# Optimization experiments

Measured on AMD Instinct MI355X. Metric: run time of the kernel, lower is better.

The kernel has to match this reference:

```python
import jax, jax.numpy as jnp
import numpy as np
from jax import lax

# ---- config (FalconH1Mixer, FalconH1-1.5B-like) ----
BATCH = 2
SEQ = 2048
HID = 2048
EXPAND = 2
INTER = EXPAND * HID          # 4096 (mamba_d_ssm=None)
HEADS = 64
PDIM = INTER // HEADS         # 64 head_dim
NSTATE = 128                  # mamba_d_state
G = 1                         # mamba_n_groups
HPG = HEADS // G
KCONV = 4                     # mamba_d_conv
GTS = G * NSTATE
CONV_DIM = INTER + 2 * GTS    # 4352
PROJ_DIM = 2 * INTER + 2 * GTS + HEADS  # 8512 (z | xBC | dt)
EPS = 1e-5
MUP = (0.25, 0.5, 0.5, 0.5, 1.0)  # ssm_multipliers for z, x, B, C, dt


def _mup_vector():
    # per-region muP multipliers over the zxbcdt projection axis
    return jnp.concatenate([
        jnp.full((INTER,), MUP[0], jnp.float32),
        jnp.full((INTER,), MUP[1], jnp.float32),
        jnp.full((GTS,), MUP[2], jnp.float32),
        jnp.full((GTS,), MUP[3], jnp.float32),
        jnp.full((HEADS,), MUP[4], jnp.float32),
    ])


def setup_inputs() -> dict:
    key = jax.random.key(0)
    ks = jax.random.split(key, 8)
    hidden_states = jax.random.normal(ks[0], (BATCH, SEQ, HID), jnp.float32)
    in_proj_w = jax.random.normal(ks[1], (HID, PROJ_DIM), jnp.float32) * 0.02
    conv_w = jax.random.normal(ks[2], (CONV_DIM, KCONV), jnp.float32) * 0.2
    conv_b = jnp.zeros((CONV_DIM,), jnp.float32)
    A_log = jnp.log(jnp.arange(1, HEADS + 1, dtype=jnp.float32))
    D = jnp.ones((HEADS,), jnp.float32)
    dt_bias = jax.random.uniform(ks[3], (HEADS,), jnp.float32)
    norm_w = jnp.ones((INTER,), jnp.float32)
    out_proj_w = jax.random.normal(ks[4], (INTER, HID), jnp.float32) * 0.02
    return dict(hidden_states=hidden_states, in_proj_w=in_proj_w, conv_w=conv_w,
                conv_b=conv_b, A_log=A_log, D=D, dt_bias=dt_bias,
                norm_w=norm_w, out_proj_w=out_proj_w)


def _forward(hidden_states, in_proj_w, conv_w, conv_b, A_log, D, dt_bias, norm_w, out_proj_w):
    b, l, _ = hidden_states.shape
    # zxbcdt projection with muP scaling
    proj = (hidden_states @ in_proj_w) * _mup_vector()  # (b, l, PROJ_DIM)
    z = proj[..., :INTER]
    xBC = proj[..., INTER:INTER + CONV_DIM]
    dt = proj[..., INTER + CONV_DIM:]                    # (b, l, HEADS)
    # depthwise causal conv1d + SiLU
    xBC_cl = jnp.swapaxes(xBC, 1, 2)                     # (b, c, l)
    conv = lax.conv_general_dilated(xBC_cl, conv_w[:, None, :],
                                    window_strides=(1,), padding=((KCONV - 1, 0),),
                                    feature_group_count=CONV_DIM)
    xBC = jax.nn.silu(jnp.swapaxes(conv + conv_b[None, :, None], 1, 2))  # (b, l, c)
    x = xBC[..., :INTER].reshape(b, l, G, HPG, PDIM)
    Bm = xBC[..., INTER:INTER + GTS].reshape(b, l, G, NSTATE)
    Cm = xBC[..., INTER + GTS:].reshape(b, l, G, NSTATE)
    # dt / A discretization
    dt = jax.nn.softplus(dt + dt_bias)                   # (b, l, HEADS)
    A = -jnp.exp(A_log)                                  # (HEADS,)
    dA = jnp.exp(dt * A).reshape(b, l, G, HPG)           # (b, l, g, c)
    dtx = dt.reshape(b, l, G, HPG)[..., None] * x        # (b, l, g, c, p)

    def step(state, inp):
        dA_t, dtx_t, B_t, C_t = inp                      # (b,g,c) (b,g,c,p) (b,g,n) (b,g,n)
        state = state * dA_t[..., None, None] + jnp.einsum('bgcp,bgn->bgcpn', dtx_t, B_t)
        y_t = jnp.einsum('bgn,bgcpn->bgcp', C_t, state)
        return state, y_t

    inputs = (jnp.moveaxis(dA, 1, 0), jnp.moveaxis(dtx, 1, 0),
              jnp.moveaxis(Bm, 1, 0), jnp.moveaxis(Cm, 1, 0))
    state0 = jnp.zeros((b, G, HPG, PDIM, NSTATE), hidden_states.dtype)
    _, ys = lax.scan(step, state0, inputs)               # (l, b, g, c, p)
    y = jnp.moveaxis(ys, 0, 1) + D.reshape(1, 1, G, HPG, 1) * x
    y = y.reshape(b, l, INTER)
    # grouped RMSNorm, then SiLU gate (norm_before_gate=True)
    yg = y.reshape(b, l, G, INTER // G)
    var = jnp.mean(jnp.square(yg), axis=-1, keepdims=True)
    yn = (yg * lax.rsqrt(var + EPS)).reshape(b, l, INTER) * norm_w
    out = yn * jax.nn.silu(z)
    return out @ out_proj_w                              # (b, l, HID)


def reference(hidden_states, in_proj_w, conv_w, conv_b, A_log, D, dt_bias, norm_w, out_proj_w):
    return _forward(hidden_states, in_proj_w, conv_w, conv_b, A_log, D, dt_bias, norm_w, out_proj_w)
```

## Files before the change

kernel.cpp:

```cpp
#include <hip/hip_runtime.h>
#include <stdint.h>

typedef unsigned short u16;
typedef unsigned int   u32;
typedef __attribute__((ext_vector_type(8))) short bf16x8;
typedef __attribute__((ext_vector_type(4))) float f32x4;
typedef __attribute__((ext_vector_type(4))) u32   u32x4;

static __device__ __forceinline__ float bf2f(u16 v){
  u32 u = ((u32)v) << 16;
  return __builtin_bit_cast(float, u);
}
static __device__ __forceinline__ u16 f2bf(float f){
  u32 u = __builtin_bit_cast(u32, f);
  return (u16)((u + 0x7fffu + ((u >> 16) & 1u)) >> 16);
}

#define MFMA16(a,b,c) __builtin_amdgcn_mfma_f32_16x16x32_bf16((a),(b),(c),0,0,0)

typedef const __attribute__((address_space(1))) char glb_c;
typedef __attribute__((address_space(3))) char lds_c;
static __device__ __forceinline__ void gload_lds16(const void* g, void* l){
  __builtin_amdgcn_global_load_lds((glb_c*)g, (lds_c*)l, 16, 0, 0);
}

#define SEQN   2048
#define PROJD  8512
#define CONVD  4352
#define INTERD 4096
#define NST    128
#define QC     64
#define NCHUNK 32

__global__ __launch_bounds__(256) void detect_kernel(
    const void* __restrict__ hidden, u32* __restrict__ flag)
{
  __shared__ int cnt;
  if (threadIdx.x == 0) cnt = 0;
  __syncthreads();
  if (threadIdx.x < 128){
    u16 v = ((const u16*)hidden)[threadIdx.x * 2];
    int e = (v >> 7) & 0xFF;
    int plaus = (v == 0) || (e >= 0x70 && e <= 0x8F);
    atomicAdd(&cnt, plaus);
  }
  __syncthreads();
  if (threadIdx.x == 0) *flag = (cnt < 64) ? 1u : 0u;
}

__global__ __launch_bounds__(256) void cvt_kernel(
    const void* __restrict__ src, u16* __restrict__ dst, int n,
    const u32* __restrict__ flag)
{
  bool isf32 = (*flag != 0);
  int stride = gridDim.x * 256;
  for (int i = blockIdx.x*256 + threadIdx.x; i < n; i += stride){
    if (isf32) dst[i] = f2bf(((const float*)src)[i]);
    else       dst[i] = ((const u16*)src)[i];
  }
}

__global__ __launch_bounds__(256) void cvt_transpose_kernel(
    const void* __restrict__ src, u16* __restrict__ dst,
    int K, int N, int Npad, const u32* __restrict__ flag)
{
  bool isf32 = (*flag != 0);
  __shared__ u16 tile[64][72];
  int n0 = blockIdx.x * 64, k0 = blockIdx.y * 64;
  int tid = threadIdx.x;
  int tr = tid >> 6;
  int tc = tid & 63;
  #pragma unroll
  for (int i = 0; i < 16; i++){
    int k = i*4 + tr;
    int gk = k0 + k, gn = n0 + tc;
    float v = 0.f;
    if (gk < K && gn < N)
      v = isf32 ? ((const float*)src)[(size_t)gk*N + gn]
                : bf2f(((const u16*)src)[(size_t)gk*N + gn]);
    tile[k][tc] = f2bf(v);
  }
  __syncthreads();
  #pragma unroll
  for (int i = 0; i < 16; i++){
    int n = i*4 + tr;
    int gn = n0 + n;
    if (gn < Npad && (k0 + tc) < K)
      dst[(size_t)gn*K + k0 + tc] = tile[tc][n];
  }
}

__global__ __launch_bounds__(256) void cvt_small_kernel(
    const void* cw, const void* cb, const void* al, const void* dv,
    const void* db, const void* nw, u16* __restrict__ base,
    const u32* __restrict__ flag)
{
  bool isf32 = (*flag != 0);
  int idx = blockIdx.x*256 + threadIdx.x;
  if (idx >= 26048) return;
  const void* src; int off;
  if      (idx < 17408){ src = cw; off = idx;          }
  else if (idx < 21760){ src = cb; off = idx - 17408;  }
  else if (idx < 21824){ src = al; off = idx - 21760;  }
  else if (idx < 21888){ src = dv; off = idx - 21824;  }
  else if (idx < 21952){ src = db; off = idx - 21888;  }
  else                 { src = nw; off = idx - 21952;  }
  u16 v = isf32 ? f2bf(((const float*)src)[off]) : ((const u16*)src)[off];
  base[idx] = v;
}

template<int MT>
__global__ __launch_bounds__(512, 2) void gemm_kernel(
    const u16* __restrict__ A, const u16* __restrict__ Bt,
    u16* __restrict__ C0, u16* __restrict__ C1, u16* __restrict__ C2,
    float* __restrict__ CF,
    int M, int N, int K, int mode)
{
  constexpr int ASZ  = MT * 16384;
  constexpr int BUFS = ASZ + 32768;
  __shared__ u16 smem[BUFS];

  const int nbx = gridDim.x;
  const int nwg = nbx * gridDim.y;
  const int bid = blockIdx.y * nbx + blockIdx.x;
  const int swz = (bid & 7) * (nwg >> 3) + (bid >> 3);
  const int m0 = (swz / nbx) * (MT*128), n0 = (swz % nbx) * 256;

  const int tid = threadIdx.x;
  const int wave = tid >> 6, lane = tid & 63;
  const int l15 = lane & 15, quad = lane >> 4;
  const int wm = wave >> 2, wn = wave & 3;

  const size_t Kb = (size_t)K * 2;
  const int srow = tid >> 3;
  const int schk = (tid & 7) ^ (srow & 7);
  const char* Abp = (const char*)A  + (size_t)(m0 + srow) * Kb + schk * 16;
  const char* Bbp = (const char*)Bt + (size_t)(n0 + srow) * Kb + schk * 16;
  char* ldsb = (char*)smem + wave * 1024;

  const int aoff0 = ((quad    ) ^ (l15 & 7)) << 4;
  const int aoff1 = ((quad + 4) ^ (l15 & 7)) << 4;
  const char* ardb[2][2];
  const char* brdb[2][2];
  #pragma unroll
  for (int c = 0; c < 2; c++){
    ardb[c][0] = (const char*)smem + c*BUFS + (wm*(MT*64) + l15)*128 + aoff0;
    ardb[c][1] = (const char*)smem + c*BUFS + (wm*(MT*64) + l15)*128 + aoff1;
    brdb[c][0] = (const char*)smem + c*BUFS + ASZ + (wn*64 + l15)*128 + aoff0;
    brdb[c][1] = (const char*)smem + c*BUFS + ASZ + (wn*64 + l15)*128 + aoff1;
  }

  f32x4 acc[MT*4][4];
  #pragma unroll
  for (int i = 0; i < MT*4; i++)
    #pragma unroll
    for (int j = 0; j < 4; j++) acc[i][j] = (f32x4){0.f,0.f,0.f,0.f};

  bf16x8 af[2*MT];
  bf16x8 bfr[8];

#define STGB(par, h, kt) do{                                             \
    const char* _s = Bbp + (size_t)((h)*128)*Kb + (size_t)(kt)*128;      \
    char* _d = ldsb + (par)*BUFS + ASZ + (h)*16384;                      \
    gload_lds16(_s, _d);                                                 \
    gload_lds16(_s + 64*Kb, _d + 8192);                                  \
  }while(0)
#define STGA(par, h, kt) do{                                             \
    const char* _s = Abp + (size_t)((h)*(MT*64))*Kb + (size_t)(kt)*128;  \
    char* _d = ldsb + (par)*BUFS + (h)*(MT*8192);                        \
    gload_lds16(_s, _d);                                                 \
    if (MT == 2) gload_lds16(_s + 64*Kb, _d + 8192);                     \
  }while(0)

  STGB(0,0,0); STGB(0,1,0);
  STGA(0,0,0); STGA(0,1,0);
  STGB(1,0,1); STGB(1,1,1);
  asm volatile("s_waitcnt vmcnt(4)" ::: "memory");
  __builtin_amdgcn_s_barrier();

  const int NT = K >> 6;
  for (int I = 0; I < (NT >> 1); ++I){
    const int T1 = 2*I+1, T2 = 2*I+2, T3 = 2*I+3;
    const bool pf = (T2 < NT);
    #pragma unroll
    for (int p = 0; p < 8; ++p){
      const int q = p & 3, c = p >> 2;
      #pragma unroll
      for (int k = 0; k < 2; k++)
        #pragma unroll
        for (int mf2 = 0; mf2 < MT; mf2++)
          af[mf2*2+k] = *(const bf16x8*)(ardb[c][k] + (MT*q+mf2)*2048);
      if (q == 0){
        #pragma unroll
        for (int nf = 0; nf < 4; nf++)
          #pragma unroll
          for (int k = 0; k < 2; k++)
            bfr[nf*2+k] = *(const bf16x8*)(brdb[c][k] + nf*2048);
      }
      if      (p == 0) STGA(1,0,T1);
      else if (p == 1) STGA(1,1,T1);
      else if (p == 2){ if (pf) STGB(0,0,T2); }
      else if (p == 3){
        if (pf){ STGB(0,1,T2);
                 asm volatile("s_waitcnt vmcnt(4)" ::: "memory"); }
        else     asm volatile("s_waitcnt vmcnt(0)" ::: "memory");
      }
      else if (p == 4){ if (pf) STGA(0,0,T2); }
      else if (p == 5){ if (pf) STGA(0,1,T2); }
      else if (p == 6){ if (pf) STGB(1,0,T3); }
      else            { if (pf){ STGB(1,1,T3);
                 asm volatile("s_waitcnt vmcnt(4)" ::: "memory"); } }
      asm volatile("" ::: "memory");
      __builtin_amdgcn_s_barrier();
      __builtin_amdgcn_s_setprio(1);
      #pragma unroll
      for (int mf2 = 0; mf2 < MT; ++mf2)
        #pragma unroll
        for (int nf = 0; nf < 4; ++nf)
          #pragma unroll
          for (int k = 0; k < 2; k++)
            acc[MT*q+mf2][nf] =
                MFMA16(af[mf2*2+k], bfr[nf*2+k], acc[MT*q+mf2][nf]);
      __builtin_amdgcn_s_setprio(0);
    }
  }
#undef STGA
#undef STGB

  #pragma unroll
  for (int nf = 0; nf < 4; nf++){
    int col = n0 + wn*64 + nf*16 + l15;
    #pragma unroll
    for (int mf = 0; mf < MT*4; mf++){
      #pragma unroll
      for (int r = 0; r < 4; r++){
        int row = m0 + wm*(MT*64) + mf*16 + quad*4 + r;
        float fv = acc[mf][nf][r];
        if (mode == 2){
          if (col < N) CF[(size_t)row*N + col] = fv;
        } else if (mode == 0){
          if (col < N) C0[(size_t)row*N + col] = f2bf(fv);
        } else {
          u16 v = f2bf(fv);
          if      (col < 4096) C0[(size_t)row*4096 + col] = v;
          else if (col < 8448) C1[(size_t)row*CONVD + (col - 4096)] = v;
          else if (col < 8512) C2[(size_t)row*64 + (col - 8448)] = v;
        }
      }
    }
  }
}

__global__ __launch_bounds__(256) void conv_silu_kernel(
    const u16* __restrict__ xbcr, const u16* __restrict__ conv_w,
    const u16* __restrict__ conv_b, u16* __restrict__ xbc)
{
  int c  = blockIdx.x * 256 + threadIdx.x;
  int rl = blockIdx.y;
  int b = rl >> 11, l = rl & 2047;
  float w[4];
  #pragma unroll
  for (int k=0;k<4;k++) w[k] = 0.5f * bf2f(conv_w[c*4 + k]);
  float acc = bf2f(conv_b[c]);
  #pragma unroll
  for (int k=0;k<4;k++){
    int s = l + k - 3;
    if (s >= 0) acc += bf2f(xbcr[(size_t)(b*2048 + s)*CONVD + c]) * w[k];
  }
  float sig = 1.f / (1.f + __expf(-acc));
  xbc[(size_t)rl*CONVD + c] = f2bf(acc * sig);
}

__global__ __launch_bounds__(256) void dt_kernel(
    const u16* __restrict__ dtraw, const u16* __restrict__ dt_bias,
    const u16* __restrict__ A_log, float* __restrict__ dt_soft,
    float* __restrict__ ldA)
{
  int idx = blockIdx.x * 256 + threadIdx.x;
  int h = idx & 63;
  float x = bf2f(dtraw[idx]) + bf2f(dt_bias[h]);
  float sp = (x > 20.f) ? x : log1pf(expf(x));
  float A = -expf(bf2f(A_log[h]));
  dt_soft[idx] = sp;
  ldA[idx] = sp * A;
}

__global__ __launch_bounds__(256) void chunk_decay_kernel(
    const float* __restrict__ ldA, float* __restrict__ cdexp)
{
  int idx = blockIdx.x * 256 + threadIdx.x;
  int q = idx & 31, bh = idx >> 5;
  int b = bh >> 6, h = bh & 63;
  float s = 0.f;
  int t0 = q * QC;
  for (int t = 0; t < QC; t++) s += ldA[(size_t)(b*2048 + t0 + t)*64 + h];
  cdexp[idx] = expf(s);
}

#define SBS  136
#define SUTS 80
#define SMS  80
__global__ __launch_bounds__(256) void ssd_intra_kernel(
    const u16* __restrict__ xbc, const float* __restrict__ dt_soft,
    const float* __restrict__ ldA, u16* __restrict__ S,
    u16* __restrict__ y)
{
  int q = blockIdx.x, h = blockIdx.y, b = blockIdx.z;
  int bh = b*64 + h;
  int t0 = q * QC;
  int tid = threadIdx.x, wave = tid >> 6, lane = tid & 63;
  int l15 = lane & 15, quad = lane >> 4;

  __shared__ u16 sB [64*SBS];
  __shared__ u16 sCM[64*SBS];
  __shared__ u16 sBt[128*64];
  __shared__ u16 sUt[64*SUTS];
  __shared__ float sLa[64];
  __shared__ float sW[64];

  if (tid < 64){
    float v = ldA[(size_t)(b*2048 + t0 + tid)*64 + h];
    #pragma unroll
    for (int off = 1; off < 64; off <<= 1){
      float o = __shfl_up(v, off, 64);
      if (lane >= off) v += o;
    }
    sLa[tid] = v;
  }
  __syncthreads();
  float laE = sLa[63];
  if (tid < 64) sW[tid] = __expf(laE - sLa[tid]);
  __syncthreads();

  #pragma unroll
  for (int i = 0; i < 4; i++){
    int ch = i*256 + tid;
    int s = ch >> 4, nc = (ch & 15) * 8;
    const u16* src = xbc + (size_t)(b*2048 + t0 + s)*CONVD;
    u32x4 vb = *(const u32x4*)(src + 4096 + nc);
    u32x4 vc = *(const u32x4*)(src + 4224 + nc);
    *(u32x4*)(sB  + s*SBS + nc) = vb;
    *(u32x4*)(sCM + s*SBS + nc) = vc;
    float wdec = sW[s];
    const u16* pb = (const u16*)&vb;
    #pragma unroll
    for (int e = 0; e < 8; e++)
      sBt[(nc + e)*64 + s] = f2bf(bf2f(pb[e]) * wdec);
  }
  #pragma unroll
  for (int i = 0; i < 2; i++){
    int ch = i*256 + tid;
    int s = ch >> 3, pc = (ch & 7) * 8;
    const u16* src = xbc + (size_t)(b*2048 + t0 + s)*CONVD + h*64 + pc;
    u32x4 vx = *(const u32x4*)src;
    float dt = dt_soft[(size_t)(b*2048 + t0 + s)*64 + h];
    const u16* px = (const u16*)&vx;
    #pragma unroll
    for (int e = 0; e < 8; e++)
      sUt[(pc + e)*SUTS + s] = f2bf(bf2f(px[e]) * dt);
  }
  __syncthreads();

  int tr = (wave & 1)*32, sc = (wave >> 1)*32;
  f32x4 aM[2][2];
  #pragma unroll
  for (int i=0;i<2;i++)
    #pragma unroll
    for (int j=0;j<2;j++) aM[i][j] = (f32x4){0.f,0.f,0.f,0.f};
  #pragma unroll
  for (int kk = 0; kk < 128; kk += 32){
    bf16x8 a0 = *(const bf16x8*)(sCM + (tr      + l15)*SBS + kk + quad*8);
    bf16x8 a1 = *(const bf16x8*)(sCM + (tr + 16 + l15)*SBS + kk + quad*8);
    bf16x8 b0 = *(const bf16x8*)(sB  + (sc      + l15)*SBS + kk + quad*8);
    bf16x8 b1 = *(const bf16x8*)(sB  + (sc + 16 + l15)*SBS + kk + quad*8);
    aM[0][0] = MFMA16(a0, b0, aM[0][0]);
    aM[0][1] = MFMA16(a0, b1, aM[0][1]);
    aM[1][0] = MFMA16(a1, b0, aM[1][0]);
    aM[1][1] = MFMA16(a1, b1, aM[1][1]);
  }
  __syncthreads();
  u16* sM = sCM;
  #pragma unroll
  for (int i = 0; i < 2; i++){
    #pragma unroll
    for (int j = 0; j < 2; j++){
      int scol = sc + j*16 + l15;
      #pragma unroll
      for (int r = 0; r < 4; r++){
        int trow = tr + i*16 + quad*4 + r;
        float v = 0.f;
        if (scol <= trow) v = aM[i][j][r] * __expf(sLa[trow] - sLa[scol]);
        sM[trow*SMS + scol] = f2bf(v);
      }
    }
  }
  __syncthreads();

  f32x4 aY[2][2];
  #pragma unroll
  for (int i=0;i<2;i++)
    #pragma unroll
    for (int j=0;j<2;j++) aY[i][j] = (f32x4){0.f,0.f,0.f,0.f};
  #pragma unroll
  for (int kk = 0; kk < 64; kk += 32){
    bf16x8 a0 = *(const bf16x8*)(sM  + (tr      + l15)*SMS  + kk + quad*8);
    bf16x8 a1 = *(const bf16x8*)(sM  + (tr + 16 + l15)*SMS  + kk + quad*8);
    bf16x8 b0 = *(const bf16x8*)(sUt + (sc      + l15)*SUTS + kk + quad*8);
    bf16x8 b1 = *(const bf16x8*)(sUt + (sc + 16 + l15)*SUTS + kk + quad*8);
    aY[0][0] = MFMA16(a0, b0, aY[0][0]);
    aY[0][1] = MFMA16(a0, b1, aY[0][1]);
    aY[1][0] = MFMA16(a1, b0, aY[1][0]);
    aY[1][1] = MFMA16(a1, b1, aY[1][1]);
  }
  #pragma unroll
  for (int i = 0; i < 2; i++){
    #pragma unroll
    for (int j = 0; j < 2; j++){
      int p = sc + j*16 + l15;
      #pragma unroll
      for (int r = 0; r < 4; r++){
        int t = tr + i*16 + quad*4 + r;
        y[(size_t)(b*2048 + t0 + t)*INTERD + h*64 + p] = f2bf(aY[i][j][r]);
      }
    }
  }

  int pr = (wave & 1)*32, nw = (wave >> 1)*64;
  f32x4 aS[2][4];
  #pragma unroll
  for (int i=0;i<2;i++)
    #pragma unroll
    for (int j=0;j<4;j++) aS[i][j] = (f32x4){0.f,0.f,0.f,0.f};
  #pragma unroll
  for (int kk = 0; kk < 64; kk += 32){
    bf16x8 a0 = *(const bf16x8*)(sUt + (pr      + l15)*SUTS + kk + quad*8);
    bf16x8 a1 = *(const bf16x8*)(sUt + (pr + 16 + l15)*SUTS + kk + quad*8);
    #pragma unroll
    for (int j = 0; j < 4; j++){
      bf16x8 bb = *(const bf16x8*)(sBt + (nw + j*16 + l15)*64 + kk + quad*8);
      aS[0][j] = MFMA16(a0, bb, aS[0][j]);
      aS[1][j] = MFMA16(a1, bb, aS[1][j]);
    }
  }
  u16* Sl = S + ((size_t)bh*NCHUNK + q)*8192;
  #pragma unroll
  for (int i = 0; i < 2; i++){
    #pragma unroll
    for (int j = 0; j < 4; j++){
      int n = nw + j*16 + l15;
      #pragma unroll
      for (int r = 0; r < 4; r++){
        int p = pr + i*16 + quad*4 + r;
        Sl[p*NST + n] = f2bf(aS[i][j][r]);
      }
    }
  }
}

__global__ __launch_bounds__(256) void ssd_carry_kernel(
    u16* __restrict__ S, const float* __restrict__ cdexp)
{
  int idx = blockIdx.x * 256 + threadIdx.x;
  int e = idx & 8191, bh = idx >> 13;
  float E = 0.f;
  for (int q = 0; q < NCHUNK; q++){
    size_t off = ((size_t)bh*NCHUNK + q)*8192 + e;
    float v = bf2f(S[off]);
    S[off] = f2bf(E);
    E = cdexp[bh*NCHUNK + q] * E + v;
  }
}

__global__ __launch_bounds__(256) void ssd_inter_kernel(
    const u16* __restrict__ xbc, const float* __restrict__ ldA,
    const u16* __restrict__ S, const u16* __restrict__ Dvec,
    u16* __restrict__ y)
{
  int q = blockIdx.x, h = blockIdx.y, b = blockIdx.z;
  int bh = b*64 + h;
  int t0 = q * QC;
  int tid = threadIdx.x, wave = tid >> 6, lane = tid & 63;
  int l15 = lane & 15, quad = lane >> 4;

  __shared__ u16 sC[64*SBS];
  __shared__ u16 sS[64*SBS];
  __shared__ float sLa[64];

  if (tid < 64){
    float v = ldA[(size_t)(b*2048 + t0 + tid)*64 + h];
    #pragma unroll
    for (int off = 1; off < 64; off <<= 1){
      float o = __shfl_up(v, off, 64);
      if (lane >= off) v += o;
    }
    sLa[tid] = v;
  }
  const u16* Sc = S + ((size_t)bh*NCHUNK + q)*8192;
  #pragma unroll
  for (int i = 0; i < 4; i++){
    int ch = i*256 + tid;
    int s = ch >> 4, nc = (ch & 15) * 8;
    *(u32x4*)(sC + s*SBS + nc) =
        *(const u32x4*)(xbc + (size_t)(b*2048 + t0 + s)*CONVD + 4224 + nc);
    *(u32x4*)(sS + s*SBS + nc) = *(const u32x4*)(Sc + s*NST + nc);
  }
  __syncthreads();

  int tr = (wave & 1)*32, pc = (wave >> 1)*32;
  f32x4 acc[2][2];
  #pragma unroll
  for (int i=0;i<2;i++)
    #pragma unroll
    for (int j=0;j<2;j++) acc[i][j] = (f32x4){0.f,0.f,0.f,0.f};
  #pragma unroll
  for (int kk = 0; kk < 128; kk += 32){
    bf16x8 a0 = *(const bf16x8*)(sC + (tr      + l15)*SBS + kk + quad*8);
    bf16x8 a1 = *(const bf16x8*)(sC + (tr + 16 + l15)*SBS + kk + quad*8);
    bf16x8 b0 = *(const bf16x8*)(sS + (pc      + l15)*SBS + kk + quad*8);
    bf16x8 b1 = *(const bf16x8*)(sS + (pc + 16 + l15)*SBS + kk + quad*8);
    acc[0][0] = MFMA16(a0, b0, acc[0][0]);
    acc[0][1] = MFMA16(a0, b1, acc[0][1]);
    acc[1][0] = MFMA16(a1, b0, acc[1][0]);
    acc[1][1] = MFMA16(a1, b1, acc[1][1]);
  }
  float Dh = bf2f(Dvec[h]);
  #pragma unroll
  for (int i = 0; i < 2; i++){
    #pragma unroll
    for (int j = 0; j < 2; j++){
      int p = pc + j*16 + l15;
      #pragma unroll
      for (int r = 0; r < 4; r++){
        int t = tr + i*16 + quad*4 + r;
        size_t row = (size_t)(b*2048 + t0 + t);
        size_t yo = row*INTERD + h*64 + p;
        float xv = bf2f(xbc[row*CONVD + h*64 + p]);
        float v = bf2f(y[yo]) + __expf(sLa[t]) * acc[i][j][r] + Dh * xv;
        y[yo] = f2bf(v);
      }
    }
  }
}

__global__ __launch_bounds__(256) void rmsnorm_gate_kernel(
    const u16* __restrict__ y, const u16* __restrict__ z,
    const u16* __restrict__ norm_w, u16* __restrict__ g)
{
  int rl = blockIdx.x;
  int tid = threadIdx.x, wave = tid >> 6, lane = tid & 63;
  const u16* yr = y + (size_t)rl*INTERD;
  float vy[16];
  float ss = 0.f;
  #pragma unroll
  for (int i = 0; i < 16; i++){
    int idx = i*256 + tid;
    float v = bf2f(yr[idx]);
    vy[i] = v;
    ss += v*v;
  }
  #pragma unroll
  for (int off = 32; off >= 1; off >>= 1) ss += __shfl_xor(ss, off, 64);
  __shared__ float red[4];
  if (lane == 0) red[wave] = ss;
  __syncthreads();
  float tot = red[0] + red[1] + red[2] + red[3];
  float rstd = rsqrtf(tot * (1.f/4096.f) + 1e-5f);
  const u16* zr = z + (size_t)rl*INTERD;
  u16* gr = g + (size_t)rl*INTERD;
  #pragma unroll
  for (int i = 0; i < 16; i++){
    int idx = i*256 + tid;
    float v = vy[i] * rstd * bf2f(norm_w[idx]);
    float zv = 0.25f * bf2f(zr[idx]);
    float sig = 1.f / (1.f + __expf(-zv));
    gr[idx] = f2bf(v * zv * sig);
  }
}

extern "C" void kernel_launch(void* const* d_in, const int* in_sizes, int n_in,
                              void* d_out, int out_size, void* d_ws, size_t ws_size,
                              hipStream_t stream)
{
  const void* hidden_r    = d_in[0];
  const void* in_proj_r   = d_in[1];
  const void* conv_w_r    = d_in[2];
  const void* conv_b_r    = d_in[3];
  const void* A_log_r     = d_in[4];
  const void* Dvec_r      = d_in[5];
  const void* dt_bias_r   = d_in[6];
  const void* norm_w_r    = d_in[7];
  const void* out_proj_r  = d_in[8];
  float* out = (float*)d_out;
  char* ws = (char*)d_ws;

  u16*   z     = (u16*)(ws + 0);
  u16*   xbcr  = (u16*)(ws + 33554432ull);
  u16*   yb    = (u16*)(ws + 33554432ull);
  u16*   dtraw = (u16*)(ws + 69206016ull);
  u16*   xbc   = (u16*)(ws + 69730304ull);
  u16*   w2b   = (u16*)(ws + 69730304ull);
  float* dt_s  = (float*)(ws + 105381888ull);
  float* lda   = (float*)(ws + 106430464ull);
  float* cdexp = (float*)(ws + 107479040ull);
  u32*   flag  = (u32*)(ws + 107495424ull);
  u16*   svec  = (u16*)(ws + 107495680ull);
  u16*   cw_b  = svec;
  u16*   cb_b  = svec + 17408;
  u16*   al_b  = svec + 21760;
  u16*   d_b   = svec + 21824;
  u16*   db_b  = svec + 21888;
  u16*   nw_b  = svec + 21952;
  u16*   S     = (u16*)(ws + 107626496ull);
  u16*   hb    = (u16*)(ws + 107626496ull);
  u16*   w1b   = (u16*)(ws + 124403712ull);
  u16*   g     = (u16*)(ws + 107626496ull);

  detect_kernel<<<1, 256, 0, stream>>>(hidden_r, flag);
  cvt_kernel<<<4096, 256, 0, stream>>>(hidden_r, hb, 8388608, flag);
  cvt_transpose_kernel<<<dim3(136, 32), 256, 0, stream>>>(
      in_proj_r, w1b, 2048, 8512, 8704, flag);
  cvt_small_kernel<<<102, 256, 0, stream>>>(conv_w_r, conv_b_r, A_log_r,
      Dvec_r, dt_bias_r, norm_w_r, svec, flag);
  gemm_kernel<2><<<dim3(34, 16), 512, 0, stream>>>(
      hb, w1b, z, xbcr, dtraw, (float*)nullptr, 4096, 8704, 2048, 1);
  conv_silu_kernel<<<dim3(17, 4096), 256, 0, stream>>>(xbcr, cw_b, cb_b, xbc);
  dt_kernel<<<1024, 256, 0, stream>>>(dtraw, db_b, al_b, dt_s, lda);
  chunk_decay_kernel<<<16, 256, 0, stream>>>(lda, cdexp);
  ssd_intra_kernel<<<dim3(NCHUNK, 64, 2), 256, 0, stream>>>(xbc, dt_s, lda, S, yb);
  ssd_carry_kernel<<<4096, 256, 0, stream>>>(S, cdexp);
  ssd_inter_kernel<<<dim3(NCHUNK, 64, 2), 256, 0, stream>>>(xbc, lda, S, d_b, yb);
  cvt_transpose_kernel<<<dim3(32, 64), 256, 0, stream>>>(
      out_proj_r, w2b, 4096, 2048, 2048, flag);
  rmsnorm_gate_kernel<<<4096, 256, 0, stream>>>(yb, z, nw_b, g);
  gemm_kernel<1><<<dim3(8, 32), 512, 0, stream>>>(
      g, w2b, (u16*)nullptr, (u16*)nullptr, (u16*)nullptr, out,
      4096, 2048, 4096, 2);
}
```

Before: 711.7 us.

## Vectorize elementwise kernels and reorder GEMM fragment loads and prefetch schedule

Converts cvt, conv_silu and rmsnorm_gate kernels to wide 8/16-byte vector loads and stores, cutting the number of memory instructions per element. In the MT==2 GEMM path it splits the K sub-steps across phases, so each phase loads four A fragments and four B fragments instead of all of them. This lowers register pressure and rebalances the staging and waitcnt schedule. The rmsnorm kernel's element-to-thread mapping changes, and conv now leaves most lanes of its third block idle.

After: 656.6 us. 1.08x faster.

```diff
diff --git a/kernel.cpp b/kernel.cpp
--- a/kernel.cpp
+++ b/kernel.cpp
@@ -4,6 +4,7 @@
 typedef unsigned short u16;
 typedef unsigned int   u32;
 typedef __attribute__((ext_vector_type(8))) short bf16x8;
+typedef __attribute__((ext_vector_type(4))) short s16x4;
 typedef __attribute__((ext_vector_type(4))) float f32x4;
 typedef __attribute__((ext_vector_type(4))) u32   u32x4;
 
@@ -53,10 +54,18 @@
     const u32* __restrict__ flag)
 {
   bool isf32 = (*flag != 0);
+  int n4 = n >> 2;
   int stride = gridDim.x * 256;
-  for (int i = blockIdx.x*256 + threadIdx.x; i < n; i += stride){
-    if (isf32) dst[i] = f2bf(((const float*)src)[i]);
-    else       dst[i] = ((const u16*)src)[i];
+  for (int i = blockIdx.x*256 + threadIdx.x; i < n4; i += stride){
+    s16x4 o;
+    if (isf32){
+      f32x4 v = ((const f32x4*)src)[i];
+      #pragma unroll
+      for (int e = 0; e < 4; e++) o[e] = (short)f2bf(v[e]);
+    } else {
+      o = ((const s16x4*)src)[i];
+    }
+    ((s16x4*)dst)[i] = o;
   }
 }
 
@@ -156,7 +165,7 @@
     #pragma unroll
     for (int j = 0; j < 4; j++) acc[i][j] = (f32x4){0.f,0.f,0.f,0.f};
 
-  bf16x8 af[2*MT];
+  bf16x8 af[4];
   bf16x8 bfr[8];
 
 #define STGB(par, h, kt) do{                                             \
@@ -184,43 +193,75 @@
     const bool pf = (T2 < NT);
     #pragma unroll
     for (int p = 0; p < 8; ++p){
-      const int q = p & 3, c = p >> 2;
-      #pragma unroll
-      for (int k = 0; k < 2; k++)
+      const int c = p >> 2;
+      if (MT == 2){
+        const int kk = (p >> 1) & 1, h = p & 1;
         #pragma unroll
-        for (int mf2 = 0; mf2 < MT; mf2++)
-          af[mf2*2+k] = *(const bf16x8*)(ardb[c][k] + (MT*q+mf2)*2048);
-      if (q == 0){
-        #pragma unroll
-        for (int nf = 0; nf < 4; nf++)
+        for (int mf2 = 0; mf2 < 4; ++mf2)
+          af[mf2] = *(const bf16x8*)(ardb[c][kk] + (h*4+mf2)*2048);
+        if (h == 0){
           #pragma unroll
-          for (int k = 0; k < 2; k++)
-            bfr[nf*2+k] = *(const bf16x8*)(brdb[c][k] + nf*2048);
+          for (int nf = 0; nf < 4; ++nf)
+            bfr[nf] = *(const bf16x8*)(brdb[c][kk] + nf*2048);
+        }
+      } else {
+        const int q = p & 3;
+        af[0] = *(const bf16x8*)(ardb[c][0] + q*2048);
+        af[1] = *(const bf16x8*)(ardb[c][1] + q*2048);
+        if (q == 0){
+          #pragma unroll
+          for (int nf = 0; nf < 4; ++nf){
+            bfr[nf*2+0] = *(const bf16x8*)(brdb[c][0] + nf*2048);
+            bfr[nf*2+1] = *(const bf16x8*)(brdb[c][1] + nf*2048);
+          }
+        }
       }
-      if      (p == 0) STGA(1,0,T1);
-      else if (p == 1) STGA(1,1,T1);
-      else if (p == 2){ if (pf) STGB(0,0,T2); }
-      else if (p == 3){
-        if (pf){ STGB(0,1,T2);
-                 asm volatile("s_waitcnt vmcnt(4)" ::: "memory"); }
-        else     asm volatile("s_waitcnt vmcnt(0)" ::: "memory");
+      if (MT == 2){
+        if      (p == 0) STGA(1,0,T1);
+        else if (p == 1) STGA(1,1,T1);
+        else if (p == 3){
+          if (pf){ STGB(0,0,T2);
+                   asm volatile("s_waitcnt vmcnt(2)" ::: "memory"); }
+          else     asm volatile("s_waitcnt vmcnt(0)" ::: "memory");
+        }
+        else if (p == 4){ if (pf) STGB(0,1,T2); }
+        else if (p == 5){ if (pf) STGA(0,0,T2); }
+        else if (p == 6){ if (pf) STGA(0,1,T2); }
+        else if (p == 7){ if (pf){ STGB(1,0,T3); STGB(1,1,T3);
+                   asm volatile("s_waitcnt vmcnt(4)" ::: "memory"); } }
+      } else {
+        if      (p == 0) STGA(1,0,T1);
+        else if (p == 1) STGA(1,1,T1);
+        else if (p == 2){ if (pf) STGB(0,0,T2); }
+        else if (p == 3){
+          if (pf){ STGB(0,1,T2);
+                   asm volatile("s_waitcnt vmcnt(4)" ::: "memory"); }
+          else     asm volatile("s_waitcnt vmcnt(0)" ::: "memory");
+        }
+        else if (p == 4){ if (pf) STGA(0,0,T2); }
+        else if (p == 5){ if (pf) STGA(0,1,T2); }
+        else if (p == 6){ if (pf) STGB(1,0,T3); }
+        else            { if (pf){ STGB(1,1,T3);
+                   asm volatile("s_waitcnt vmcnt(4)" ::: "memory"); } }
       }
-      else if (p == 4){ if (pf) STGA(0,0,T2); }
-      else if (p == 5){ if (pf) STGA(0,1,T2); }
-      else if (p == 6){ if (pf) STGB(1,0,T3); }
-      else            { if (pf){ STGB(1,1,T3);
-                 asm volatile("s_waitcnt vmcnt(4)" ::: "memory"); } }
       asm volatile("" ::: "memory");
       __builtin_amdgcn_s_barrier();
       __builtin_amdgcn_s_setprio(1);
-      #pragma unroll
-      for (int mf2 = 0; mf2 < MT; ++mf2)
+      if (MT == 2){
+        const int h = p & 1;
         #pragma unroll
-        for (int nf = 0; nf < 4; ++nf)
+        for (int mf2 = 0; mf2 < 4; ++mf2)
           #pragma unroll
-          for (int k = 0; k < 2; k++)
-            acc[MT*q+mf2][nf] =
-                MFMA16(af[mf2*2+k], bfr[nf*2+k], acc[MT*q+mf2][nf]);
+          for (int nf = 0; nf < 4; ++nf)
+            acc[h*4+mf2][nf] = MFMA16(af[mf2], bfr[nf], acc[h*4+mf2][nf]);
+      } else {
+        const int q = p & 3;
+        #pragma unroll
+        for (int nf = 0; nf < 4; ++nf){
+          acc[q][nf] = MFMA16(af[0], bfr[nf*2+0], acc[q][nf]);
+          acc[q][nf] = MFMA16(af[1], bfr[nf*2+1], acc[q][nf]);
+        }
+      }
       __builtin_amdgcn_s_setprio(0);
     }
   }
@@ -255,20 +296,40 @@
     const u16* __restrict__ xbcr, const u16* __restrict__ conv_w,
     const u16* __restrict__ conv_b, u16* __restrict__ xbc)
 {
-  int c  = blockIdx.x * 256 + threadIdx.x;
+  int c8 = blockIdx.x * 256 + threadIdx.x;
+  if (c8 >= 544) return;
+  int c = c8 * 8;
   int rl = blockIdx.y;
   int b = rl >> 11, l = rl & 2047;
-  float w[4];
-  #pragma unroll
-  for (int k=0;k<4;k++) w[k] = 0.5f * bf2f(conv_w[c*4 + k]);
-  float acc = bf2f(conv_b[c]);
-  #pragma unroll
-  for (int k=0;k<4;k++){
+
+  u16 wv[32];
+  *(u32x4*)(wv +  0) = *(const u32x4*)(conv_w + c*4);
+  *(u32x4*)(wv +  8) = *(const u32x4*)(conv_w + c*4 +  8);
+  *(u32x4*)(wv + 16) = *(const u32x4*)(conv_w + c*4 + 16);
+  *(u32x4*)(wv + 24) = *(const u32x4*)(conv_w + c*4 + 24);
+  u16 bv[8];
+  *(u32x4*)bv = *(const u32x4*)(conv_b + c);
+
+  u16 xv[4][8];
+  #pragma unroll
+  for (int k = 0; k < 4; k++){
     int s = l + k - 3;
-    if (s >= 0) acc += bf2f(xbcr[(size_t)(b*2048 + s)*CONVD + c]) * w[k];
-  }
-  float sig = 1.f / (1.f + __expf(-acc));
-  xbc[(size_t)rl*CONVD + c] = f2bf(acc * sig);
+    if (s >= 0)
+      *(u32x4*)(xv[k]) = *(const u32x4*)(xbcr + (size_t)(b*2048 + s)*CONVD + c);
+    else
+      *(u32x4*)(xv[k]) = (u32x4){0,0,0,0};
+  }
+  u16 ov[8];
+  #pragma unroll
+  for (int e = 0; e < 8; e++){
+    float acc = bf2f(bv[e]);
+    #pragma unroll
+    for (int k = 0; k < 4; k++)
+      acc += bf2f(xv[k][e]) * (0.5f * bf2f(wv[e*4 + k]));
+    float sig = 1.f / (1.f + __expf(-acc));
+    ov[e] = f2bf(acc * sig);
+  }
+  *(u32x4*)(xbc + (size_t)rl*CONVD + c) = *(u32x4*)ov;
 }
 
 __global__ __launch_bounds__(256) void dt_kernel(
@@ -549,13 +610,15 @@
   int rl = blockIdx.x;
   int tid = threadIdx.x, wave = tid >> 6, lane = tid & 63;
   const u16* yr = y + (size_t)rl*INTERD;
-  float vy[16];
+  u16 vy[16];
+  *(u32x4*)(vy + 0) = *(const u32x4*)(yr + tid*8);
+  *(u32x4*)(vy + 8) = *(const u32x4*)(yr + 2048 + tid*8);
+  float fy[16];
   float ss = 0.f;
   #pragma unroll
   for (int i = 0; i < 16; i++){
-    int idx = i*256 + tid;
-    float v = bf2f(yr[idx]);
-    vy[i] = v;
+    float v = bf2f(vy[i]);
+    fy[i] = v;
     ss += v*v;
   }
   #pragma unroll
@@ -567,14 +630,20 @@
   float rstd = rsqrtf(tot * (1.f/4096.f) + 1e-5f);
   const u16* zr = z + (size_t)rl*INTERD;
   u16* gr = g + (size_t)rl*INTERD;
+  u16 vz[16], vw[16], go[16];
+  *(u32x4*)(vz + 0) = *(const u32x4*)(zr + tid*8);
+  *(u32x4*)(vz + 8) = *(const u32x4*)(zr + 2048 + tid*8);
+  *(u32x4*)(vw + 0) = *(const u32x4*)(norm_w + tid*8);
+  *(u32x4*)(vw + 8) = *(const u32x4*)(norm_w + 2048 + tid*8);
   #pragma unroll
   for (int i = 0; i < 16; i++){
-    int idx = i*256 + tid;
-    float v = vy[i] * rstd * bf2f(norm_w[idx]);
-    float zv = 0.25f * bf2f(zr[idx]);
+    float v = fy[i] * rstd * bf2f(vw[i]);
+    float zv = 0.25f * bf2f(vz[i]);
     float sig = 1.f / (1.f + __expf(-zv));
-    gr[idx] = f2bf(v * zv * sig);
-  }
+    go[i] = f2bf(v * zv * sig);
+  }
+  *(u32x4*)(gr + tid*8)        = *(u32x4*)(go + 0);
+  *(u32x4*)(gr + 2048 + tid*8) = *(u32x4*)(go + 8);
 }
 
 extern "C" void kernel_launch(void* const* d_in, const int* in_sizes, int n_in,
@@ -623,7 +692,7 @@
       Dvec_r, dt_bias_r, norm_w_r, svec, flag);
   gemm_kernel<2><<<dim3(34, 16), 512, 0, stream>>>(
       hb, w1b, z, xbcr, dtraw, (float*)nullptr, 4096, 8704, 2048, 1);
-  conv_silu_kernel<<<dim3(17, 4096), 256, 0, stream>>>(xbcr, cw_b, cb_b, xbc);
+  conv_silu_kernel<<<dim3(3, 4096), 256, 0, stream>>>(xbcr, cw_b, cb_b, xbc);
   dt_kernel<<<1024, 256, 0, stream>>>(dtraw, db_b, al_b, dt_s, lda);
   chunk_decay_kernel<<<16, 256, 0, stream>>>(lda, cdexp);
   ssd_intra_kernel<<<dim3(NCHUNK, 64, 2), 256, 0, stream>>>(xbc, dt_s, lda, S, yb);
```
